# Kernel tuning notes

Measured on AMD Instinct MI355X. Metric: run time of the kernel, lower is better.

## Reference

```python
import jax, jax.numpy as jnp
import numpy as np

DIM = 1024
HEADS = 16
DIM_HEAD = 64
INNER = HEADS * DIM_HEAD  # 1024
SCALE = DIM_HEAD ** -0.5


def setup_inputs() -> dict:
    key = jax.random.key(0)
    k_x, k_qkv, k_out, k_g, k_b = jax.random.split(key, 5)
    x = jax.random.normal(k_x, (4, 2048, DIM), dtype=jnp.float32)
    # LayerNorm affine params (torch default: weight=1, bias=0; keep learnable-shaped)
    ln_gamma = jnp.ones((DIM,), dtype=jnp.float32)
    ln_beta = jnp.zeros((DIM,), dtype=jnp.float32)
    w_qkv = jax.random.normal(k_qkv, (DIM, 3 * INNER), dtype=jnp.float32) * (DIM ** -0.5)
    w_out = jax.random.normal(k_out, (INNER, DIM), dtype=jnp.float32) * (INNER ** -0.5)
    return {"x": x, "ln_gamma": ln_gamma, "ln_beta": ln_beta, "w_qkv": w_qkv, "w_out": w_out}


def reference(x, ln_gamma, ln_beta, w_qkv, w_out):
    # LayerNorm (eps matches torch default 1e-5)
    mu = jnp.mean(x, axis=-1, keepdims=True)
    var = jnp.mean(jnp.square(x - mu), axis=-1, keepdims=True)
    xn = (x - mu) * jax.lax.rsqrt(var + 1e-5) * ln_gamma + ln_beta

    qkv = xn @ w_qkv  # [b, n, 3*inner]
    q, k, v = jnp.split(qkv, 3, axis=-1)

    def to_heads(t):  # b n (h d) -> b h n d
        b, n, _ = t.shape
        return t.reshape(b, n, HEADS, DIM_HEAD).transpose(0, 2, 1, 3)

    q, k, v = to_heads(q), to_heads(k), to_heads(v)

    dots = jnp.einsum('bhid,bhjd->bhij', q, k) * SCALE  # [b,h,n,n]
    attn = jax.nn.softmax(dots, axis=-1)
    out = jnp.einsum('bhij,bhjd->bhid', attn, v)  # [b,h,n,d]

    b, h, n, d = out.shape
    out = out.transpose(0, 2, 1, 3).reshape(b, n, h * d)  # b h n d -> b n (h d)
    return out @ w_out
```

## Files before the change

### kernel.cpp

```cpp
#include <hip/hip_runtime.h>

#define DIM 1024
#define HEADS 16
#define DHEAD 64
#define SEQ 2048
#define BATCH 4
#define ROWS (BATCH*SEQ)
#define QK_COLS (3*DIM)
#define QSCALE 0.18033688011112042f

typedef __bf16 bf16x8 __attribute__((ext_vector_type(8)));
typedef __bf16 bf16x4 __attribute__((ext_vector_type(4)));
typedef short s16x4 __attribute__((ext_vector_type(4)));
typedef float f32x4 __attribute__((ext_vector_type(4)));
typedef unsigned short u16;
typedef unsigned int u32;

__device__ __forceinline__ u16 f2bf(float f) {
  u32 u = __float_as_uint(f);
  u = (u + 0x7fffu + ((u >> 16) & 1u)) >> 16;
  return (u16)u;
}

__device__ __forceinline__ void gld16(const void* g, void* s) {
  __builtin_amdgcn_global_load_lds((__attribute__((address_space(1))) void*)g,
                                   (__attribute__((address_space(3))) void*)s, 16, 0, 0);
}

__device__ __forceinline__ float fexp2(float x) {
#if defined(__HIP_DEVICE_COMPILE__)
  return __builtin_amdgcn_exp2f(x);
#else
  return x;
#endif
}

__device__ __forceinline__ s16x4 pack_bf16(f32x4 v) {
  bf16x4 b = __builtin_convertvector(v, bf16x4);
  union { bf16x4 b; s16x4 s; } u; u.b = b; return u.s;
}

__global__ __launch_bounds__(256) void prep_kernel(
    const float* __restrict__ x, const float* __restrict__ gam, const float* __restrict__ bet,
    u16* __restrict__ xn,
    const float* __restrict__ wqkv, u16* __restrict__ wqkvT,
    const float* __restrict__ wout, u16* __restrict__ woutT) {
  __shared__ float tile[32][33];
  int bid = blockIdx.x, tid = threadIdx.x;
  if (bid < ROWS) {
    int lane = tid & 63, w = tid >> 6;
    const float4 xv = *(const float4*)(x + (size_t)bid*DIM + tid*4);
    float s = xv.x + xv.y + xv.z + xv.w;
    float q = xv.x*xv.x + xv.y*xv.y + xv.z*xv.z + xv.w*xv.w;
    for (int off = 32; off > 0; off >>= 1) { s += __shfl_xor(s, off, 64); q += __shfl_xor(q, off, 64); }
    float* red = &tile[0][0];
    if (lane == 0) { red[w] = s; red[4+w] = q; }
    __syncthreads();
    s = red[0]+red[1]+red[2]+red[3];
    q = red[4]+red[5]+red[6]+red[7];
    float mean = s * (1.0f/DIM);
    float rstd = rsqrtf(q*(1.0f/DIM) - mean*mean + 1e-5f);
    float4 gv = *(const float4*)(gam + tid*4);
    float4 bv = *(const float4*)(bet + tid*4);
    ushort4 o;
    o.x = f2bf((xv.x-mean)*rstd*gv.x + bv.x);
    o.y = f2bf((xv.y-mean)*rstd*gv.y + bv.y);
    o.z = f2bf((xv.z-mean)*rstd*gv.z + bv.z);
    o.w = f2bf((xv.w-mean)*rstd*gv.w + bv.w);
    *(ushort4*)(xn + (size_t)bid*DIM + tid*4) = o;
  } else {
    const float* in; u16* out; int R, C, c0, r0;
    if (bid < ROWS + 3072) {
      int t = bid - ROWS;
      in = wqkv; out = wqkvT; R = DIM; C = QK_COLS;
      c0 = (t % 96) * 32; r0 = (t / 96) * 32;
    } else {
      int t = bid - ROWS - 3072;
      in = wout; out = woutT; R = DIM; C = DIM;
      c0 = (t & 31) * 32; r0 = (t >> 5) * 32;
    }
    int tx = tid & 31, ty = tid >> 5;
    for (int i = 0; i < 32; i += 8)
      tile[ty+i][tx] = in[(size_t)(r0+ty+i)*C + c0 + tx];
    __syncthreads();
    for (int i = 0; i < 32; i += 8)
      out[(size_t)(c0+ty+i)*R + r0 + tx] = f2bf(tile[tx][ty+i]);
  }
}

template<int NOUT, int EPI>
__global__ __launch_bounds__(256, 2) void gemm_bt(const u16* __restrict__ A, const u16* __restrict__ Bt,
                                                  void* __restrict__ Cv, u16* __restrict__ vT, int K) {
  __shared__ alignas(16) u16 smem[24576];
  int tid = threadIdx.x;
  int lane = tid & 63, w = tid >> 6;
  int l = lane & 15, quad = lane >> 4;
  int wm = (w & 1) * 64, wn = (w >> 1) * 64;
  int m0 = blockIdx.y * 128, n0 = blockIdx.x * 128;
  const u16* Ag = A + (size_t)m0 * K;
  const u16* Bg = Bt + (size_t)n0 * K;
  bool sw = (EPI == 1) || (n0 < 2048);
  f32x4 z = {0.f, 0.f, 0.f, 0.f};
  f32x4 acc[4][4];
  for (int i = 0; i < 4; ++i) for (int j = 0; j < 4; ++j) acc[i][j] = z;

  #pragma unroll
  for (int c = 0; c < 2; ++c) {
    int idx = c*256 + tid;
    int row = idx >> 2, col = (idx & 3) << 3;
    gld16(Ag + (size_t)row*K + col, smem + idx*8);
    gld16(Bg + (size_t)row*K + col, smem + 4096 + idx*8);
  }
  #pragma unroll
  for (int c = 0; c < 2; ++c) {
    int idx = c*256 + tid;
    int row = idx >> 2, col = (idx & 3) << 3;
    gld16(Ag + (size_t)row*K + 32 + col, smem + 8192 + idx*8);
    gld16(Bg + (size_t)row*K + 32 + col, smem + 12288 + idx*8);
  }

  int NT = K >> 5;
  int ca = 0, cb = 8192, cc = 16384;
  for (int kt = 0; kt < NT; ++kt) {
    __builtin_amdgcn_sched_barrier(0);
    if (kt < NT - 1) __asm__ volatile("s_waitcnt vmcnt(4)" ::: "memory");
    else             __asm__ volatile("s_waitcnt vmcnt(0)" ::: "memory");
    __builtin_amdgcn_s_barrier();
    __builtin_amdgcn_sched_barrier(0);
    const u16* As = smem + ca;
    const u16* Bs = As + 4096;
    if (kt + 2 < NT) {
      u16* dst = (u16*)smem + cc;
      int ko = (kt+2)*32;
      #pragma unroll
      for (int c = 0; c < 2; ++c) {
        int idx = c*256 + tid;
        int row = idx >> 2, col = (idx & 3) << 3;
        gld16(Ag + (size_t)row*K + ko + col, dst + idx*8);
        gld16(Bg + (size_t)row*K + ko + col, dst + 4096 + idx*8);
      }
    }
    bf16x8 af[4], bfr[4];
    #pragma unroll
    for (int t = 0; t < 4; ++t) {
      af[t]  = *(const bf16x8*)(As + (wm + t*16 + l)*32 + quad*8);
      bfr[t] = *(const bf16x8*)(Bs + (wn + t*16 + l)*32 + quad*8);
    }
    if (sw) {
      #pragma unroll
      for (int i = 0; i < 4; ++i)
        #pragma unroll
        for (int j = 0; j < 4; ++j)
          acc[i][j] = __builtin_amdgcn_mfma_f32_16x16x32_bf16(bfr[i], af[j], acc[i][j], 0, 0, 0);
    } else {
      #pragma unroll
      for (int i = 0; i < 4; ++i)
        #pragma unroll
        for (int j = 0; j < 4; ++j)
          acc[i][j] = __builtin_amdgcn_mfma_f32_16x16x32_bf16(af[i], bfr[j], acc[i][j], 0, 0, 0);
    }
    int tr = ca; ca = cb; cb = cc; cc = tr;
  }

  if (EPI == 0) {
    u16* C = (u16*)Cv;
    int region = n0 >> 10;
    if (region == 0) {
      for (int i = 0; i < 4; ++i)
        for (int j = 0; j < 4; ++j) {
          int nq = n0 + wn + i*16 + quad*4;
          int m  = m0 + wm + j*16 + l;
          f32x4 v = acc[i][j] * QSCALE;
          *(s16x4*)(C + (size_t)m*QK_COLS + nq) = pack_bf16(v);
        }
    } else if (region == 1) {
      for (int i = 0; i < 4; ++i)
        for (int j = 0; j < 4; ++j) {
          int nq = n0 + wn + i*16 + quad*4;
          int m  = m0 + wm + j*16 + l;
          int d  = nq & 63;
          int col = (nq & ~63) | ((((d >> 3) ^ (m & 7)) << 3) | (d & 7));
          *(s16x4*)(C + (size_t)m*QK_COLS + col) = pack_bf16(acc[i][j]);
        }
    } else {
      for (int i = 0; i < 4; ++i)
        for (int j = 0; j < 4; ++j) {
          int mrow = m0 + wm + i*16 + quad*4;
          int hd   = (n0 - 2048) + wn + j*16 + l;
          int h = hd >> 6, d = hd & 63;
          int bb = mrow >> 11, nloc = mrow & 2047;
          int jloc = nloc & 31;
          int hi = jloc >> 4;
          int u  = ((nloc >> 5) & 3) * 4 + ((jloc >> 2) & 3);
          int c16 = u ^ (d & 15);
          int p = (nloc & ~127) | (c16 << 3) | (hi << 2);
          *(s16x4*)(vT + ((size_t)(bb*16 + h)*DHEAD + d)*SEQ + p) = pack_bf16(acc[i][j]);
        }
    }
  } else {
    float* C = (float*)Cv;
    for (int i = 0; i < 4; ++i)
      for (int j = 0; j < 4; ++j) {
        int n = n0 + wn + i*16 + quad*4;
        int m = m0 + wm + j*16 + l;
        *(f32x4*)(C + (size_t)m*NOUT + n) = acc[i][j];
      }
  }
}

__global__ __launch_bounds__(256, 2) void attn_kernel(const u16* __restrict__ qkv,
    const u16* __restrict__ vT, u16* __restrict__ aout) {
  __shared__ alignas(16) u16 smem[32768];
  int tid = threadIdx.x;
  int lane = tid & 63, w = tid >> 6;
  int l = lane & 15, quad = lane >> 4;
  int bh = blockIdx.x, qt = blockIdx.y;
  int b = bh >> 4, h = bh & 15;
  int qrow0 = b*SEQ + qt*128;

  bf16x8 aq[2][2];
  #pragma unroll
  for (int mt = 0; mt < 2; ++mt)
    #pragma unroll
    for (int ks = 0; ks < 2; ++ks)
      aq[mt][ks] = *(const bf16x8*)(qkv + (size_t)(qrow0 + w*32 + mt*16 + l)*QK_COLS + h*DHEAD + ks*32 + quad*8);

  f32x4 z = {0.f,0.f,0.f,0.f};
  f32x4 o[4][2];
  #pragma unroll
  for (int dt = 0; dt < 4; ++dt) for (int mt = 0; mt < 2; ++mt) o[dt][mt] = z;
  f32x4 psum[2] = {z, z};

  const u16* kbase = qkv + (size_t)b*SEQ*QK_COLS + DIM + h*DHEAD;
  const u16* vbase = vT + (size_t)bh*DHEAD*SEQ;

  #pragma unroll
  for (int c = 0; c < 4; ++c) {
    int idx = c*256 + tid;
    gld16(kbase + (size_t)(idx >> 3)*QK_COLS + ((idx & 7) << 3), smem + idx*8);
    gld16(vbase + (size_t)(idx >> 4)*SEQ + ((idx & 15) << 3), smem + 8192 + idx*8);
  }

  for (int kt = 0; kt < 16; ++kt) {
    __syncthreads();
    const u16* Kt = smem + (kt & 1)*16384;
    const u16* Vt = Kt + 8192;
    if (kt < 15) {
      u16* dst = (u16*)smem + ((kt+1) & 1)*16384;
      int krow0 = (kt+1)*128;
      #pragma unroll
      for (int c = 0; c < 4; ++c) {
        int idx = c*256 + tid;
        gld16(kbase + (size_t)(krow0 + (idx >> 3))*QK_COLS + ((idx & 7) << 3), dst + idx*8);
        gld16(vbase + (size_t)(idx >> 4)*SEQ + krow0 + ((idx & 15) << 3), dst + 8192 + idx*8);
      }
    }

    s16x4 pb[2][8];
    #pragma unroll
    for (int jt = 0; jt < 8; ++jt) {
      bf16x8 bk0 = *(const bf16x8*)(Kt + (jt*16 + l)*64 + (((0*4 + quad) ^ (l & 7)) << 3));
      bf16x8 bk1 = *(const bf16x8*)(Kt + (jt*16 + l)*64 + (((1*4 + quad) ^ (l & 7)) << 3));
      #pragma unroll
      for (int mt = 0; mt < 2; ++mt) {
        f32x4 st = __builtin_amdgcn_mfma_f32_16x16x32_bf16(bk0, aq[mt][0], z, 0,0,0);
        st = __builtin_amdgcn_mfma_f32_16x16x32_bf16(bk1, aq[mt][1], st, 0,0,0);
        f32x4 p;
        p[0] = fexp2(st[0]); p[1] = fexp2(st[1]);
        p[2] = fexp2(st[2]); p[3] = fexp2(st[3]);
        psum[mt] += p;
        pb[mt][jt] = pack_bf16(p);
      }
    }

    #pragma unroll
    for (int jb = 0; jb < 4; ++jb) {
      union { s16x4 h[2]; bf16x8 v; } p0, p1;
      p0.h[0] = pb[0][2*jb]; p0.h[1] = pb[0][2*jb+1];
      p1.h[0] = pb[1][2*jb]; p1.h[1] = pb[1][2*jb+1];
      #pragma unroll
      for (int dt = 0; dt < 4; ++dt) {
        int d = dt*16 + l;
        bf16x8 av = *(const bf16x8*)(Vt + d*128 + (((jb*4 + quad) ^ l) << 3));
        o[dt][0] = __builtin_amdgcn_mfma_f32_16x16x32_bf16(av, p0.v, o[dt][0], 0,0,0);
        o[dt][1] = __builtin_amdgcn_mfma_f32_16x16x32_bf16(av, p1.v, o[dt][1], 0,0,0);
      }
    }
  }

  float li[2];
  #pragma unroll
  for (int mt = 0; mt < 2; ++mt) {
    float ps = psum[mt][0] + psum[mt][1] + psum[mt][2] + psum[mt][3];
    ps += __shfl_xor(ps, 16, 64);
    ps += __shfl_xor(ps, 32, 64);
    li[mt] = ps;
  }

  __syncthreads();
  u16* Ep = smem + w*2304;
  #pragma unroll
  for (int mt = 0; mt < 2; ++mt) {
    float inv = 1.0f / li[mt];
    #pragma unroll
    for (int dt = 0; dt < 4; ++dt)
      #pragma unroll
      for (int r = 0; r < 4; ++r)
        Ep[(mt*16 + l)*72 + dt*16 + quad*4 + r] = f2bf(o[dt][mt][r] * inv);
  }
  __asm__ volatile("s_waitcnt lgkmcnt(0)" ::: "memory");
  int lr = lane >> 1, half = lane & 1;
  size_t grow = (size_t)qrow0 + w*32 + lr;
  #pragma unroll
  for (int k = 0; k < 4; ++k) {
    uint4 vv = *(const uint4*)(Ep + lr*72 + half*32 + k*8);
    *(uint4*)(aout + grow*DIM + h*DHEAD + half*32 + k*8) = vv;
  }
}

extern "C" void kernel_launch(void* const* d_in, const int* in_sizes, int n_in,
                              void* d_out, int out_size, void* d_ws, size_t ws_size,
                              hipStream_t stream) {
  const float* x    = (const float*)d_in[0];
  const float* gam  = (const float*)d_in[1];
  const float* bet  = (const float*)d_in[2];
  const float* wqkv = (const float*)d_in[3];
  const float* wout = (const float*)d_in[4];
  float* out = (float*)d_out;

  u16* xn    = (u16*)d_ws;
  u16* wqkvT = xn    + (size_t)ROWS*DIM;
  u16* woutT = wqkvT + (size_t)QK_COLS*DIM;
  u16* qkvb  = woutT + (size_t)DIM*DIM;
  u16* vTb   = qkvb  + (size_t)ROWS*QK_COLS;
  u16* aoutb = vTb   + (size_t)64*DHEAD*SEQ;

  prep_kernel<<<ROWS + 3072 + 1024, 256, 0, stream>>>(x, gam, bet, xn, wqkv, wqkvT, wout, woutT);
  gemm_bt<QK_COLS,0><<<dim3(QK_COLS/128, ROWS/128), 256, 0, stream>>>(xn, wqkvT, (void*)qkvb, vTb, DIM);
  attn_kernel<<<dim3(64, SEQ/128), 256, 0, stream>>>(qkvb, vTb, aoutb);
  gemm_bt<DIM,1><<<dim3(DIM/128, ROWS/128), 256, 0, stream>>>(aoutb, woutT, (void*)out, nullptr, DIM);
}
```

Before: 267.6 us.

## Use BK=64 double-buffered GEMM with XOR-swizzled LDS layout

Replaces the 3-stage, BK=32 LDS pipeline in the projection GEMM with a 2-stage pipeline that loads 64-wide K tiles, using XOR swizzling of 16-byte chunks to avoid LDS bank conflicts. Each iteration runs two MFMA k-substeps, which halves the number of barriers per K. Shared memory grows to 64KB per block, which may limit occupancy at 2 blocks per CU. The new loop replaces the explicit vmcnt waits with __syncthreads, so less prefetch distance is kept in flight.

```diff
diff --git a/kernel.cpp b/kernel.cpp
--- a/kernel.cpp
+++ b/kernel.cpp
@@ -91,7 +91,7 @@
 template<int NOUT, int EPI>
 __global__ __launch_bounds__(256, 2) void gemm_bt(const u16* __restrict__ A, const u16* __restrict__ Bt,
                                                   void* __restrict__ Cv, u16* __restrict__ vT, int K) {
-  __shared__ alignas(16) u16 smem[24576];
+  __shared__ alignas(16) u16 smem[32768];
   int tid = threadIdx.x;
   int lane = tid & 63, w = tid >> 6;
   int l = lane & 15, quad = lane >> 4;
@@ -104,63 +104,53 @@
   f32x4 acc[4][4];
   for (int i = 0; i < 4; ++i) for (int j = 0; j < 4; ++j) acc[i][j] = z;
 
-  #pragma unroll
-  for (int c = 0; c < 2; ++c) {
-    int idx = c*256 + tid;
-    int row = idx >> 2, col = (idx & 3) << 3;
-    gld16(Ag + (size_t)row*K + col, smem + idx*8);
-    gld16(Bg + (size_t)row*K + col, smem + 4096 + idx*8);
-  }
-  #pragma unroll
-  for (int c = 0; c < 2; ++c) {
-    int idx = c*256 + tid;
-    int row = idx >> 2, col = (idx & 3) << 3;
-    gld16(Ag + (size_t)row*K + 32 + col, smem + 8192 + idx*8);
-    gld16(Bg + (size_t)row*K + 32 + col, smem + 12288 + idx*8);
-  }
-
-  int NT = K >> 5;
-  int ca = 0, cb = 8192, cc = 16384;
+  #define STG(dstOff, srcG, ko) do { \
+    _Pragma("unroll") \
+    for (int c_ = 0; c_ < 4; ++c_) { \
+      int idx_ = c_*256 + tid; \
+      int row_ = idx_ >> 3, cc_ = idx_ & 7; \
+      gld16((srcG) + (size_t)row_*K + (ko) + ((cc_ ^ (row_ & 7)) << 3), \
+            smem + (dstOff) + idx_*8); \
+    } } while (0)
+
+  STG(0, Ag, 0);
+  STG(8192, Bg, 0);
+
+  int NT = K >> 6;
   for (int kt = 0; kt < NT; ++kt) {
-    __builtin_amdgcn_sched_barrier(0);
-    if (kt < NT - 1) __asm__ volatile("s_waitcnt vmcnt(4)" ::: "memory");
-    else             __asm__ volatile("s_waitcnt vmcnt(0)" ::: "memory");
-    __builtin_amdgcn_s_barrier();
-    __builtin_amdgcn_sched_barrier(0);
-    const u16* As = smem + ca;
-    const u16* Bs = As + 4096;
-    if (kt + 2 < NT) {
-      u16* dst = (u16*)smem + cc;
-      int ko = (kt+2)*32;
-      #pragma unroll
-      for (int c = 0; c < 2; ++c) {
-        int idx = c*256 + tid;
-        int row = idx >> 2, col = (idx & 3) << 3;
-        gld16(Ag + (size_t)row*K + ko + col, dst + idx*8);
-        gld16(Bg + (size_t)row*K + ko + col, dst + 4096 + idx*8);
-      }
-    }
-    bf16x8 af[4], bfr[4];
-    #pragma unroll
-    for (int t = 0; t < 4; ++t) {
-      af[t]  = *(const bf16x8*)(As + (wm + t*16 + l)*32 + quad*8);
-      bfr[t] = *(const bf16x8*)(Bs + (wn + t*16 + l)*32 + quad*8);
-    }
-    if (sw) {
-      #pragma unroll
-      for (int i = 0; i < 4; ++i)
+    __syncthreads();
+    const u16* As = smem + (kt & 1)*16384;
+    const u16* Bs = As + 8192;
+    if (kt + 1 < NT) {
+      int dstOff = ((kt+1) & 1)*16384;
+      int ko = (kt+1)*64;
+      STG(dstOff, Ag, ko);
+      STG(dstOff + 8192, Bg, ko);
+    }
+    #pragma unroll
+    for (int ks = 0; ks < 2; ++ks) {
+      bf16x8 af[4], bfr[4];
+      #pragma unroll
+      for (int t = 0; t < 4; ++t) {
+        af[t]  = *(const bf16x8*)(As + (wm + t*16 + l)*64 + (((ks*4 + quad) ^ (l & 7)) << 3));
+        bfr[t] = *(const bf16x8*)(Bs + (wn + t*16 + l)*64 + (((ks*4 + quad) ^ (l & 7)) << 3));
+      }
+      if (sw) {
         #pragma unroll
-        for (int j = 0; j < 4; ++j)
-          acc[i][j] = __builtin_amdgcn_mfma_f32_16x16x32_bf16(bfr[i], af[j], acc[i][j], 0, 0, 0);
-    } else {
-      #pragma unroll
-      for (int i = 0; i < 4; ++i)
+        for (int i = 0; i < 4; ++i)
+          #pragma unroll
+          for (int j = 0; j < 4; ++j)
+            acc[i][j] = __builtin_amdgcn_mfma_f32_16x16x32_bf16(bfr[i], af[j], acc[i][j], 0, 0, 0);
+      } else {
         #pragma unroll
-        for (int j = 0; j < 4; ++j)
-          acc[i][j] = __builtin_amdgcn_mfma_f32_16x16x32_bf16(af[i], bfr[j], acc[i][j], 0, 0, 0);
-    }
-    int tr = ca; ca = cb; cb = cc; cc = tr;
-  }
+        for (int i = 0; i < 4; ++i)
+          #pragma unroll
+          for (int j = 0; j < 4; ++j)
+            acc[i][j] = __builtin_amdgcn_mfma_f32_16x16x32_bf16(af[i], bfr[j], acc[i][j], 0, 0, 0);
+      }
+    }
+  }
+  #undef STG
 
   if (EPI == 0) {
     u16* C = (u16*)Cv;
```

Result: faster. 246.4 us (-7.9%).
